# Kernel optimization log

Measured on AMD Instinct MI355X. Metric: run time of the kernel, lower is better.

## Reference

```python
import jax, jax.numpy as jnp
import numpy as np

B, CIN, COUT, H, W, KH, KW, G = 16, 64, 128, 128, 128, 3, 3, 4


def setup_inputs() -> dict:
    key = jax.random.key(0)
    k1, k2, k3 = jax.random.split(key, 3)
    x = jax.random.normal(k1, (B, CIN, H, W), dtype=jnp.float32)
    spline_weights = jax.random.normal(k2, (COUT, CIN, KH, KW, G), dtype=jnp.float32)
    basis_weights = jax.random.normal(k3, (COUT, CIN, KH, KW), dtype=jnp.float32)
    return {"x": x, "spline_weights": spline_weights, "basis_weights": basis_weights}


def _conv_same(inp, w):
    # NCHW x OIHW -> NCHW, stride 1, SAME padding (pad = k//2, matches torch F.pad)
    return jax.lax.conv_general_dilated(
        inp, w, window_strides=(1, 1),
        padding=[(KH // 2, KH // 2), (KW // 2, KW // 2)],
        dimension_numbers=("NCHW", "OIHW", "NCHW"))


def reference(x, spline_weights, basis_weights):
    # spline branch: patch broadcast over grid then summed == conv with grid-summed kernel
    w_spline = spline_weights.sum(axis=-1)  # (COUT, CIN, KH, KW)
    # basis branch: silu applied to (zero-)padded patches; silu(0)=0 so equals conv(silu(x))
    return _conv_same(x, w_spline) + _conv_same(jax.nn.silu(x), basis_weights)
```

## Files before the change

### kernel.cpp

```cpp
#include <hip/hip_runtime.h>
#include <math.h>

#define B_    16
#define CIN   64
#define COUT  128
#define H_    128
#define W_    128
#define CI2   128
#define KTOT  1152

typedef __bf16 bf16x8 __attribute__((ext_vector_type(8)));
typedef float  f32x4  __attribute__((ext_vector_type(4)));

#define XT_BYTES  ((size_t)B_ * H_ * W_ * CI2 * 2)
#define WC_BYTES  ((size_t)COUT * KTOT * 2)
#define Z_OFF     (XT_BYTES + WC_BYTES)
#define WS_NEED   (Z_OFF + 4096)

__global__ __launch_bounds__(256) void w_prep(const float* __restrict__ sw,
                                              const float* __restrict__ bw,
                                              __bf16* __restrict__ wc,
                                              float* __restrict__ zp) {
    const int i = blockIdx.x * 256 + threadIdx.x;
    if (blockIdx.x == 0) zp[threadIdx.x] = 0.f;
    if (i >= COUT * KTOT) return;
    const int co = i / KTOT, k = i - co * KTOT;
    const int tap = k >> 7, ci2 = k & 127;
    float v;
    if (ci2 < CIN) {
        const float* p = sw + ((size_t)(co * CIN + ci2) * 9 + tap) * 4;
        v = p[0] + p[1] + p[2] + p[3];
    } else {
        v = bw[(size_t)(co * CIN + (ci2 - CIN)) * 9 + tap];
    }
    const int wm = co >> 6, m = (co >> 4) & 3, l15 = co & 15;
    const int ks = (k >> 5) & 3, lq = (k >> 3) & 3, e = k & 7;
    const int hh = tap * 2 + (ks >> 1);
    const int f  = (wm * 4 + m) * 2 + (ks & 1);
    const size_t off = ((size_t)(hh * 16 + f)) * 512 + (lq * 16 + l15) * 8 + e;
    wc[off] = (__bf16)v;
}

__global__ __launch_bounds__(256) void xt_prep(const float* __restrict__ x,
                                               __bf16* __restrict__ xt) {
    __shared__ __align__(16) __bf16 tile[64][136];
    const int t  = threadIdx.x;
    const int w0 = blockIdx.x * 64;
    const int h  = blockIdx.y;
    const int b  = blockIdx.z;
    const float* xb = x + ((size_t)(b * CIN) * H_ + h) * W_ + w0;
#pragma unroll
    for (int rep = 0; rep < 16; ++rep) {
        const int idx = rep * 256 + t;
        const int ci = idx >> 6, w = idx & 63;
        const float v = xb[(size_t)ci * H_ * W_ + w];
        tile[w][ci]       = (__bf16)v;
        tile[w][CIN + ci] = (__bf16)(v / (1.f + __expf(-v)));
    }
    __syncthreads();
    __bf16* ob = xt + (((size_t)b * H_ + h) * W_ + w0) * CI2;
#pragma unroll
    for (int rep = 0; rep < 4; ++rep) {
        const int idx = rep * 256 + t;
        const int w = idx >> 4, sl = idx & 15;
        *(bf16x8*)(ob + (size_t)w * CI2 + sl * 8) = *(const bf16x8*)(&tile[w][sl * 8]);
    }
}

__global__ __launch_bounds__(256, 2) void kan_mfma(const __bf16* __restrict__ xt,
                                                   const __bf16* __restrict__ wc,
                                                   const float* __restrict__ zp,
                                                   float* __restrict__ out) {
    __shared__ __align__(16) char xs[2880 * 16];
    __shared__ __align__(16) char asA[1024 * 16];
    __shared__ __align__(16) char asB[1024 * 16];
    const int t    = threadIdx.x;
    const int lane = t & 63, wave = t >> 6;
    const int wm = wave >> 1, wn = wave & 1;
    const int l15 = lane & 15, lq = lane >> 4;

    const int orig = blockIdx.x;
    const int wid  = (orig & 7) * 256 + (orig >> 3);
    const int b  = wid >> 7;
    const int hy = (wid & 127) >> 3, wx = wid & 7;
    const int w0 = wx * 16, h0 = hy * 8;

    const size_t xbase = (size_t)b * (H_ * W_ * CI2);
#pragma unroll
    for (int i = 0; i < 12; ++i) {
        const int s = i * 256 + t;
        if (s < 2880) {
            const int pos = s >> 4, q = s & 15;
            const int ih = pos / 18, iw = pos - ih * 18;
            const int gh = h0 + ih - 1, gw = w0 + iw - 1;
            const int chunk = q ^ (pos & 15);
            const void* src;
            if (gh >= 0 && gh < H_ && gw >= 0 && gw < W_)
                src = (const void*)(xt + xbase + ((size_t)(gh * W_ + gw)) * CI2 + chunk * 8);
            else
                src = (const void*)zp;
            __builtin_amdgcn_global_load_lds(
                (const __attribute__((address_space(1))) unsigned int*)src,
                (__attribute__((address_space(3))) unsigned int*)(xs + s * 16), 16, 0, 0);
        }
    }

#define STAGEH_(buf, hh)                                                        \
    _Pragma("unroll")                                                           \
    for (int i = 0; i < 4; ++i) {                                               \
        const int s = i * 256 + t;                                              \
        __builtin_amdgcn_global_load_lds(                                       \
            (const __attribute__((address_space(1))) unsigned int*)              \
                (wc + (size_t)(hh) * 8192 + s * 8),                             \
            (__attribute__((address_space(3))) unsigned int*)((buf) + s * 16),  \
            16, 0, 0);                                                          \
    }

#define COMPUTE2_(buf, kss)                                                     \
    _Pragma("unroll")                                                           \
    for (int k2 = 0; k2 < 2; ++k2) {                                            \
        const int ks = (kss) + k2;                                              \
        bf16x8 af[4], bfr[4];                                                   \
        _Pragma("unroll")                                                       \
        for (int m = 0; m < 4; ++m)                                             \
            af[m] = *(const bf16x8*)((buf) +                                    \
                ((wm * 4 + m) * 2 + (ks & 1)) * 1024 + lane * 16);              \
        _Pragma("unroll")                                                       \
        for (int n = 0; n < 4; ++n) {                                           \
            const int pos_ = pos0[n] + dpos;                                    \
            const int swz_ = (ks * 4 + lq) ^ (pos_ & 15);                       \
            bfr[n] = *(const bf16x8*)(xs + pos_ * 256 + swz_ * 16);             \
        }                                                                       \
        _Pragma("unroll")                                                       \
        for (int m = 0; m < 4; ++m)                                             \
            _Pragma("unroll")                                                   \
            for (int n = 0; n < 4; ++n)                                         \
                acc[m][n] = __builtin_amdgcn_mfma_f32_16x16x32_bf16(            \
                    af[m], bfr[n], acc[m][n], 0, 0, 0);                         \
    }

    STAGEH_(asA, 0);
    __syncthreads();

    f32x4 acc[4][4] = {};
    int pos0[4];
#pragma unroll
    for (int n = 0; n < 4; ++n) pos0[n] = (wn * 4 + n) * 18 + l15;

#pragma unroll 1
    for (int tap = 0; tap < 9; ++tap) {
        const int kh = (tap * 11) >> 5;
        const int kw = tap - kh * 3;
        const int dpos = kh * 18 + kw;

        STAGEH_(asB, tap * 2 + 1);
        COMPUTE2_(asA, 0);
        __syncthreads();

        if (tap < 8) STAGEH_(asA, tap * 2 + 2);
        COMPUTE2_(asB, 2);
        __syncthreads();
    }

    float* ob = out + (size_t)b * COUT * H_ * W_;
#pragma unroll
    for (int m = 0; m < 4; ++m) {
        const int co = wm * 64 + m * 16 + lq * 4;
#pragma unroll
        for (int n = 0; n < 4; ++n) {
            const int ph = wn * 4 + n;
            float* p = ob + ((size_t)co * H_ + (h0 + ph)) * W_ + (w0 + l15);
#pragma unroll
            for (int r = 0; r < 4; ++r)
                p[(size_t)r * H_ * W_] = acc[m][n][r];
        }
    }
#undef STAGEH_
#undef COMPUTE2_
}

#define TS   16
#define COB  8
#define TIN  18
__global__ __launch_bounds__(256) void spline_sum_kernel(const float* __restrict__ sw,
                                                         float* __restrict__ wsum) {
    int i = blockIdx.x * 256 + threadIdx.x;
    if (i < COUT * CIN * 9) {
        const float4 v = *reinterpret_cast<const float4*>(sw + (size_t)i * 4);
        wsum[i] = v.x + v.y + v.z + v.w;
    }
}
__global__ __launch_bounds__(256) void kan_conv(const float* __restrict__ x,
                                                const float* __restrict__ wsp,
                                                const float* __restrict__ wb,
                                                float* __restrict__ out) {
    __shared__ float xsm[TIN][20];
    __shared__ float ssm[TIN][20];
    const int t = threadIdx.x, tx = t & 15, ty = t >> 4;
    const int w0 = (blockIdx.x & 7) * TS, h0 = (blockIdx.x >> 3) * TS;
    const int co0 = blockIdx.y * COB, b = blockIdx.z;
    float acc[COB];
#pragma unroll
    for (int i = 0; i < COB; ++i) acc[i] = 0.f;
    const float* xb = x + (size_t)b * CIN * H_ * W_;
    for (int ci = 0; ci < CIN; ++ci) {
        __syncthreads();
        const float* xc = xb + (size_t)ci * H_ * W_;
        for (int p = t; p < TIN * TIN; p += 256) {
            int r = p / TIN, c = p - r * TIN;
            int ih = h0 + r - 1, iw = w0 + c - 1;
            float v = 0.f;
            if (ih >= 0 && ih < H_ && iw >= 0 && iw < W_) v = xc[ih * W_ + iw];
            xsm[r][c] = v;
            ssm[r][c] = v / (1.f + expf(-v));
        }
        __syncthreads();
        float xv[9], sv[9];
#pragma unroll
        for (int kh = 0; kh < 3; ++kh)
#pragma unroll
            for (int kw = 0; kw < 3; ++kw) {
                xv[kh * 3 + kw] = xsm[ty + kh][tx + kw];
                sv[kh * 3 + kw] = ssm[ty + kh][tx + kw];
            }
#pragma unroll
        for (int co = 0; co < COB; ++co) {
            const float* w1 = wsp + ((size_t)(co0 + co) * CIN + ci) * 9;
            const float* w2 = wb  + ((size_t)(co0 + co) * CIN + ci) * 9;
#pragma unroll
            for (int k = 0; k < 9; ++k)
                acc[co] += xv[k] * w1[k] + sv[k] * w2[k];
        }
    }
    const int oh = h0 + ty, ow = w0 + tx;
#pragma unroll
    for (int co = 0; co < COB; ++co)
        out[(((size_t)b * COUT + (co0 + co)) * H_ + oh) * W_ + ow] = acc[co];
}

extern "C" void kernel_launch(void* const* d_in, const int* in_sizes, int n_in,
                              void* d_out, int out_size, void* d_ws, size_t ws_size,
                              hipStream_t stream) {
    const float* x  = (const float*)d_in[0];
    const float* sw = (const float*)d_in[1];
    const float* bw = (const float*)d_in[2];
    float* out = (float*)d_out;

    if (ws_size >= WS_NEED) {
        __bf16* xt = (__bf16*)d_ws;
        __bf16* wc = (__bf16*)((char*)d_ws + XT_BYTES);
        float*  zp = (float*)((char*)d_ws + Z_OFF);
        w_prep<<<(COUT * KTOT + 255) / 256, 256, 0, stream>>>(sw, bw, wc, zp);
        xt_prep<<<dim3(2, H_, B_), 256, 0, stream>>>(x, xt);
        kan_mfma<<<dim3(2048), 256, 0, stream>>>(xt, wc, zp, out);
    } else {
        float* wsum = (float*)d_ws;
        spline_sum_kernel<<<(COUT * CIN * 9 + 255) / 256, 256, 0, stream>>>(sw, wsum);
        kan_conv<<<dim3(64, COUT / COB, B_), 256, 0, stream>>>(x, wsum, bw, out);
    }
}
```

Measured before the change: 114.7 us.

## Split input halo staging by channel half to cut LDS and raise occupancy

The MFMA conv kernel now stages the input halo in two channel halves (64 channels each) instead of all 128 at once. This halves the halo LDS buffer and shrinks the weight stage buffers, so launch bounds can target three blocks per CU instead of two. The weight layout in w_prep is reordered to match the new K-step order, and B fragments are prefetched into registers one step ahead, with s_setprio raised around the MFMA bursts. In exchange the kernel adds an extra halo reload with two more barriers, smaller pipeline stages, more loop iterations, and higher register pressure from the prefetched fragments.

```diff
diff --git a/kernel.cpp b/kernel.cpp
--- a/kernel.cpp
+++ b/kernel.cpp
@@ -34,10 +34,10 @@
         v = bw[(size_t)(co * CIN + (ci2 - CIN)) * 9 + tap];
     }
     const int wm = co >> 6, m = (co >> 4) & 3, l15 = co & 15;
-    const int ks = (k >> 5) & 3, lq = (k >> 3) & 3, e = k & 7;
-    const int hh = tap * 2 + (ks >> 1);
-    const int f  = (wm * 4 + m) * 2 + (ks & 1);
-    const size_t off = ((size_t)(hh * 16 + f)) * 512 + (lq * 16 + l15) * 8 + e;
+    const int ks = ci2 >> 5, lq = (ci2 >> 3) & 3, e = ci2 & 7;
+    const int qq = (ks >> 1) * 18 + tap * 2 + (ks & 1);
+    const int f  = wm * 4 + m;
+    const size_t off = ((size_t)(qq * 8 + f)) * 512 + (lq * 16 + l15) * 8 + e;
     wc[off] = (__bf16)v;
 }
 
@@ -67,13 +67,13 @@
     }
 }
 
-__global__ __launch_bounds__(256, 2) void kan_mfma(const __bf16* __restrict__ xt,
+__global__ __launch_bounds__(256, 3) void kan_mfma(const __bf16* __restrict__ xt,
                                                    const __bf16* __restrict__ wc,
                                                    const float* __restrict__ zp,
                                                    float* __restrict__ out) {
-    __shared__ __align__(16) char xs[2880 * 16];
-    __shared__ __align__(16) char asA[1024 * 16];
-    __shared__ __align__(16) char asB[1024 * 16];
+    __shared__ __align__(16) char bh[1440 * 16];
+    __shared__ __align__(16) char asA[512 * 16];
+    __shared__ __align__(16) char asB[512 * 16];
     const int t    = threadIdx.x;
     const int lane = t & 63, wave = t >> 6;
     const int wm = wave >> 1, wn = wave & 1;
@@ -86,80 +86,100 @@
     const int w0 = wx * 16, h0 = hy * 8;
 
     const size_t xbase = (size_t)b * (H_ * W_ * CI2);
-#pragma unroll
-    for (int i = 0; i < 12; ++i) {
-        const int s = i * 256 + t;
-        if (s < 2880) {
-            const int pos = s >> 4, q = s & 15;
-            const int ih = pos / 18, iw = pos - ih * 18;
-            const int gh = h0 + ih - 1, gw = w0 + iw - 1;
-            const int chunk = q ^ (pos & 15);
-            const void* src;
-            if (gh >= 0 && gh < H_ && gw >= 0 && gw < W_)
-                src = (const void*)(xt + xbase + ((size_t)(gh * W_ + gw)) * CI2 + chunk * 8);
-            else
-                src = (const void*)zp;
-            __builtin_amdgcn_global_load_lds(
-                (const __attribute__((address_space(1))) unsigned int*)src,
-                (__attribute__((address_space(3))) unsigned int*)(xs + s * 16), 16, 0, 0);
-        }
-    }
-
-#define STAGEH_(buf, hh)                                                        \
+
+#define STAGEB_(kk)                                                             \
     _Pragma("unroll")                                                           \
-    for (int i = 0; i < 4; ++i) {                                               \
+    for (int i = 0; i < 6; ++i) {                                               \
+        const int s = i * 256 + t;                                              \
+        if (s < 1440) {                                                         \
+            const int pos = s >> 3, q = s & 7;                                  \
+            const int ih = pos / 18, iw = pos - ih * 18;                        \
+            const int gh = h0 + ih - 1, gw = w0 + iw - 1;                       \
+            const int chunk = q ^ (pos & 7);                                    \
+            const void* src;                                                    \
+            if (gh >= 0 && gh < H_ && gw >= 0 && gw < W_)                       \
+                src = (const void*)(xt + xbase +                                \
+                      ((size_t)(gh * W_ + gw)) * CI2 + (kk) * 64 + chunk * 8);  \
+            else                                                                \
+                src = (const void*)zp;                                          \
+            __builtin_amdgcn_global_load_lds(                                   \
+                (const __attribute__((address_space(1))) unsigned int*)src,     \
+                (__attribute__((address_space(3))) unsigned int*)(bh + s * 16), \
+                16, 0, 0);                                                      \
+        }                                                                       \
+    }
+
+#define STAGEQ_(buf, qq)                                                        \
+    _Pragma("unroll")                                                           \
+    for (int i = 0; i < 2; ++i) {                                               \
         const int s = i * 256 + t;                                              \
         __builtin_amdgcn_global_load_lds(                                       \
             (const __attribute__((address_space(1))) unsigned int*)              \
-                (wc + (size_t)(hh) * 8192 + s * 8),                             \
+                (wc + (size_t)(qq) * 4096 + s * 8),                             \
             (__attribute__((address_space(3))) unsigned int*)((buf) + s * 16),  \
             16, 0, 0);                                                          \
     }
 
-#define COMPUTE2_(buf, kss)                                                     \
-    _Pragma("unroll")                                                           \
-    for (int k2 = 0; k2 < 2; ++k2) {                                            \
-        const int ks = (kss) + k2;                                              \
-        bf16x8 af[4], bfr[4];                                                   \
+#define LOADB1_(dst, tp, ksl)                                                   \
+    {                                                                           \
+        const int kh_ = ((tp) * 11) >> 5;                                       \
+        const int dp_ = kh_ * 18 + ((tp) - kh_ * 3);                            \
+        _Pragma("unroll")                                                       \
+        for (int n = 0; n < 4; ++n) {                                           \
+            const int pos_ = pos0[n] + dp_;                                     \
+            const int swz_ = ((ksl) * 4 + lq) ^ (pos_ & 7);                     \
+            dst[n] = *(const bf16x8*)(bh + pos_ * 128 + swz_ * 16);             \
+        }                                                                       \
+    }
+
+#define COMPUTE1_(buf, bfr)                                                     \
+    {                                                                           \
+        bf16x8 af[4];                                                           \
         _Pragma("unroll")                                                       \
         for (int m = 0; m < 4; ++m)                                             \
-            af[m] = *(const bf16x8*)((buf) +                                    \
-                ((wm * 4 + m) * 2 + (ks & 1)) * 1024 + lane * 16);              \
-        _Pragma("unroll")                                                       \
-        for (int n = 0; n < 4; ++n) {                                           \
-            const int pos_ = pos0[n] + dpos;                                    \
-            const int swz_ = (ks * 4 + lq) ^ (pos_ & 15);                       \
-            bfr[n] = *(const bf16x8*)(xs + pos_ * 256 + swz_ * 16);             \
-        }                                                                       \
+            af[m] = *(const bf16x8*)((buf) + (wm * 4 + m) * 1024 + lane * 16);  \
+        __builtin_amdgcn_s_setprio(1);                                          \
         _Pragma("unroll")                                                       \
         for (int m = 0; m < 4; ++m)                                             \
             _Pragma("unroll")                                                   \
             for (int n = 0; n < 4; ++n)                                         \
                 acc[m][n] = __builtin_amdgcn_mfma_f32_16x16x32_bf16(            \
                     af[m], bfr[n], acc[m][n], 0, 0, 0);                         \
-    }
-
-    STAGEH_(asA, 0);
-    __syncthreads();
+        __builtin_amdgcn_s_setprio(0);                                          \
+    }
 
     f32x4 acc[4][4] = {};
     int pos0[4];
 #pragma unroll
     for (int n = 0; n < 4; ++n) pos0[n] = (wn * 4 + n) * 18 + l15;
 
+    bf16x8 bP[4], bQ[4];
+
+    STAGEB_(0);
+    STAGEQ_(asA, 0);
+    __syncthreads();
+    LOADB1_(bP, 0, 0);
+
 #pragma unroll 1
-    for (int tap = 0; tap < 9; ++tap) {
-        const int kh = (tap * 11) >> 5;
-        const int kw = tap - kh * 3;
-        const int dpos = kh * 18 + kw;
-
-        STAGEH_(asB, tap * 2 + 1);
-        COMPUTE2_(asA, 0);
-        __syncthreads();
-
-        if (tap < 8) STAGEH_(asA, tap * 2 + 2);
-        COMPUTE2_(asB, 2);
-        __syncthreads();
+    for (int kk = 0; kk < 2; ++kk) {
+        if (kk) {
+            __syncthreads();
+            STAGEB_(1);
+            __syncthreads();
+            LOADB1_(bP, 0, 0);
+        }
+#pragma unroll 1
+        for (int tap = 0; tap < 9; ++tap) {
+            const int qq = kk * 18 + tap * 2;
+            if (qq + 1 < 36) STAGEQ_(asB, qq + 1);
+            COMPUTE1_(asA, bP);
+            LOADB1_(bQ, tap, 1);
+            __syncthreads();
+            if (qq + 2 < 36) STAGEQ_(asA, qq + 2);
+            COMPUTE1_(asB, bQ);
+            if (tap < 8) LOADB1_(bP, tap + 1, 0);
+            __syncthreads();
+        }
     }
 
     float* ob = out + (size_t)b * COUT * H_ * W_;
@@ -175,8 +195,10 @@
                 p[(size_t)r * H_ * W_] = acc[m][n][r];
         }
     }
-#undef STAGEH_
-#undef COMPUTE2_
+#undef STAGEB_
+#undef STAGEQ_
+#undef LOADB1_
+#undef COMPUTE1_
 }
 
 #define TS   16
```

After: 103.6 us. -9.7%, faster.
